# Kernel tuning notes

Hardware: AMD Instinct MI355X
Metric: run time of the kernel (lower is better)

Reference implementation:

```python
import jax, jax.numpy as jnp
import numpy as np

D = 1024        # d_model
H = 16          # query heads
HKV = 4         # kv heads (GQA)
HD = D // H     # head dim = 64
MAX_T = 1024
EPS = 1e-6
CAP = 50.0      # logit softcap


def _rope_cache(max_t, hd):
    inv = 1.0 / (10000.0 ** (np.arange(0, hd, 2, dtype=np.float32) / hd))  # (hd/2,)
    t = np.arange(max_t, dtype=np.float32)
    f = np.outer(t, inv)                                                   # (max_t, hd/2)
    return jnp.asarray(np.cos(f)), jnp.asarray(np.sin(f))


def setup_inputs() -> dict:
    key = jax.random.key(0)
    ks = jax.random.split(key, 5)
    x = jax.random.normal(ks[0], (2, 64, 256, D), jnp.float32)  # (B,T,S,D)
    wq = jax.random.normal(ks[1], (D, H * HD), jnp.float32) * 0.02
    wk = jax.random.normal(ks[2], (D, HKV * HD), jnp.float32) * 0.02
    wv = jax.random.normal(ks[3], (D, HKV * HD), jnp.float32) * 0.02
    wo = jax.random.normal(ks[4], (H * HD, D), jnp.float32) * 0.02
    q_scale = jnp.ones((HD,), jnp.float32)  # QKNorm learnable gains
    k_scale = jnp.ones((HD,), jnp.float32)
    rope_cos, rope_sin = _rope_cache(MAX_T, HD)
    return {"x": x, "wq": wq, "wk": wk, "wv": wv, "wo": wo,
            "q_scale": q_scale, "k_scale": k_scale,
            "rope_cos": rope_cos, "rope_sin": rope_sin}


def _rmsnorm(v, scale):
    return v * jax.lax.rsqrt(jnp.mean(v * v, axis=-1, keepdims=True) + EPS) * scale


def reference(x, wq, wk, wv, wo, q_scale, k_scale, rope_cos, rope_sin):
    B, T, S, Dm = x.shape
    # fold spatial positions into batch: each position attends causally over time
    xt = x.transpose(0, 2, 1, 3).reshape(B * S, T, Dm)          # (N,T,D)
    q = (xt @ wq).reshape(B * S, T, H, HD)
    k = (xt @ wk).reshape(B * S, T, HKV, HD)
    v = (xt @ wv).reshape(B * S, T, HKV, HD)
    # QK-norm (RMSNorm over head_dim) before RoPE
    q = _rmsnorm(q, q_scale)
    k = _rmsnorm(k, k_scale)
    # 1D RoPE over temporal positions (split-half convention)
    cos = rope_cos[:T][None, :, None, :]                        # (1,T,1,HD/2)
    sin = rope_sin[:T][None, :, None, :]

    def rot(u):
        u1, u2 = jnp.split(u, 2, axis=-1)
        return jnp.concatenate([u1 * cos - u2 * sin, u1 * sin + u2 * cos], axis=-1)

    q = rot(q)
    k = rot(k)
    # GQA: expand kv heads to match query heads
    rep = H // HKV
    k = jnp.repeat(k, rep, axis=2)
    v = jnp.repeat(v, rep, axis=2)
    scores = jnp.einsum('nthd,nshd->nhts', q, k) / np.float32(np.sqrt(HD))
    scores = CAP * jnp.tanh(scores / CAP)                        # logit softcap
    causal = jnp.tril(jnp.ones((T, T), bool))
    scores = jnp.where(causal, scores, jnp.float32(-1e30))
    a = jax.nn.softmax(scores, axis=-1)
    o = jnp.einsum('nhts,nshd->nthd', a, v).reshape(B * S, T, H * HD) @ wo
    return o.reshape(B, S, T, Dm).transpose(0, 2, 1, 3)          # (B,T,S,D)
```

## Files before the change

### kernel.cpp

```cpp
#include <hip/hip_runtime.h>
#include <hip/hip_bf16.h>

#define DM   1024
#define NHQ  16
#define NKVH 4
#define HDIM 64
#define TTT  64
#define SSS  256
#define NBB  2
#define MROWS 32768

using short8 = __attribute__((ext_vector_type(8))) short;
using short4v = __attribute__((ext_vector_type(4))) short;
using f32x4  = __attribute__((ext_vector_type(4))) float;

__device__ __forceinline__ short f2bf(float f) {
  union { __hip_bfloat16 h; short s; } u;
  u.h = __float2bfloat16(f);
  return u.s;
}

__device__ __forceinline__ f32x4 mfma16(short8 a, short8 b, f32x4 c) {
  return __builtin_amdgcn_mfma_f32_16x16x32_bf16(a, b, c, 0, 0, 0);
}

__device__ __forceinline__ void gload_lds16(const void* g, void* l) {
  __builtin_amdgcn_global_load_lds(
      (const __attribute__((address_space(1))) void*)g,
      (__attribute__((address_space(3))) void*)l, 16, 0, 0);
}

__global__ __launch_bounds__(256) void k_prep(const float* __restrict__ x,
                                              short* __restrict__ xb,
                                              const float* __restrict__ wq,
                                              const float* __restrict__ wk,
                                              const float* __restrict__ wv,
                                              const float* __restrict__ wo,
                                              short* __restrict__ wqkvT,
                                              short* __restrict__ woT) {
  __shared__ float tile[32][33];
  int bid = blockIdx.x;
  if (bid < 4096) {
    float4 v[8];
    #pragma unroll
    for (int i = 0; i < 8; ++i) {
      int r = bid * 8 + i;
      int n = r >> 6, t = r & 63;
      int b = n >> 8, s = n & 255;
      v[i] = ((const float4*)(x + ((size_t)((b * TTT + t) * SSS + s)) * DM))[threadIdx.x];
    }
    #pragma unroll
    for (int i = 0; i < 8; ++i) {
      int r = bid * 8 + i;
      short4 o;
      o.x = f2bf(v[i].x); o.y = f2bf(v[i].y); o.z = f2bf(v[i].z); o.w = f2bf(v[i].w);
      ((short4*)(xb + (size_t)r * DM))[threadIdx.x] = o;
    }
    return;
  }
  bid -= 4096;
  const float* w; short* wt; int cols;
  if (bid < 1024)      { w = wq; wt = wqkvT; cols = 1024; }
  else if (bid < 1280) { w = wk; wt = wqkvT + (size_t)1024 * 1024; cols = 256; bid -= 1024; }
  else if (bid < 1536) { w = wv; wt = wqkvT + (size_t)1280 * 1024; cols = 256; bid -= 1280; }
  else                 { w = wo; wt = woT; cols = 1024; bid -= 1536; }
  int ctiles = cols >> 5;
  int tj = bid % ctiles;
  int td = bid / ctiles;
  int lx = threadIdx.x & 31, ly = threadIdx.x >> 5;
  #pragma unroll
  for (int rr = 0; rr < 32; rr += 8)
    tile[rr + ly][lx] = w[(size_t)(td * 32 + rr + ly) * cols + tj * 32 + lx];
  __syncthreads();
  #pragma unroll
  for (int rr = 0; rr < 32; rr += 8)
    wt[(size_t)(tj * 32 + rr + ly) * 1024 + td * 32 + lx] = f2bf(tile[lx][rr + ly]);
}

#define TILE(RAK0, RAK1, RBK0, RBK1, NLB, CLB, G, IA, IB, VM)                  \
  {                                                                            \
    short8 a[4], b0[4], b1[4];                                                 \
    _Pragma("unroll") for (int n = 0; n < 4; ++n)                              \
        b0[n] = *(const short8*)(RBK0 + n * 1024);                             \
    _Pragma("unroll") for (int m = 0; m < 4; ++m)                              \
        a[m] = *(const short8*)(RAK0 + m * 1024);                              \
    if (IA) stA0(NLB, (G + 1) * 64);                                           \
    __builtin_amdgcn_s_barrier();                                              \
    asm volatile("s_waitcnt lgkmcnt(0)" ::: "memory");                         \
    __builtin_amdgcn_s_setprio(1);                                             \
    _Pragma("unroll") for (int m = 0; m < 4; ++m)                              \
      _Pragma("unroll") for (int n = 0; n < 4; ++n)                            \
          acc[m][n] = mfma16(a[m], b0[n], acc[m][n]);                          \
    __builtin_amdgcn_s_setprio(0);                                             \
    __builtin_amdgcn_s_barrier();                                              \
    _Pragma("unroll") for (int m = 0; m < 4; ++m)                              \
        a[m] = *(const short8*)(RAK0 + 4096 + m * 1024);                       \
    if (IA) stA1(NLB, (G + 1) * 64);                                           \
    __builtin_amdgcn_s_barrier();                                              \
    asm volatile("s_waitcnt lgkmcnt(0)" ::: "memory");                         \
    __builtin_amdgcn_s_setprio(1);                                             \
    _Pragma("unroll") for (int m = 0; m < 4; ++m)                              \
      _Pragma("unroll") for (int n = 0; n < 4; ++n)                            \
          acc[4 + m][n] = mfma16(a[m], b0[n], acc[4 + m][n]);                  \
    __builtin_amdgcn_s_setprio(0);                                             \
    __builtin_amdgcn_s_barrier();                                              \
    _Pragma("unroll") for (int n = 0; n < 4; ++n)                              \
        b1[n] = *(const short8*)(RBK1 + n * 1024);                             \
    _Pragma("unroll") for (int m = 0; m < 4; ++m)                              \
        a[m] = *(const short8*)(RAK1 + m * 1024);                              \
    __builtin_amdgcn_s_barrier();                                              \
    asm volatile("s_waitcnt lgkmcnt(0)" ::: "memory");                         \
    __builtin_amdgcn_s_setprio(1);                                             \
    _Pragma("unroll") for (int m = 0; m < 4; ++m)                              \
      _Pragma("unroll") for (int n = 0; n < 4; ++n)                            \
          acc[m][n] = mfma16(a[m], b1[n], acc[m][n]);                          \
    __builtin_amdgcn_s_setprio(0);                                             \
    __builtin_amdgcn_s_barrier();                                              \
    _Pragma("unroll") for (int m = 0; m < 4; ++m)                              \
        a[m] = *(const short8*)(RAK1 + 4096 + m * 1024);                       \
    if (IB) stB(CLB, (G + 2) * 64);                                            \
    __builtin_amdgcn_s_barrier();                                              \
    asm volatile("s_waitcnt lgkmcnt(0)" ::: "memory");                         \
    __builtin_amdgcn_s_setprio(1);                                             \
    _Pragma("unroll") for (int m = 0; m < 4; ++m)                              \
      _Pragma("unroll") for (int n = 0; n < 4; ++n)                            \
          acc[4 + m][n] = mfma16(a[m], b1[n], acc[4 + m][n]);                  \
    __builtin_amdgcn_s_setprio(0);                                             \
    if (VM == 4)      asm volatile("s_waitcnt vmcnt(4)" ::: "memory");         \
    else if (VM == 0) asm volatile("s_waitcnt vmcnt(0)" ::: "memory");         \
    __builtin_amdgcn_s_barrier();                                              \
  }

__device__ __forceinline__ void gemm256(const short* __restrict__ Ab,
                                        const short* __restrict__ Bb,
                                        short* __restrict__ sm,
                                        f32x4 (&acc)[8][4]) {
  const int tid = threadIdx.x, lane = tid & 63, wid = tid >> 6;
  const int wr = wid >> 2, wc = wid & 3;
  const int ln15 = lane & 15, lhi = lane >> 4;
  const int rsw = ln15 & 7;
  const int row_t = tid >> 3;
  const int sw = ((tid & 7) ^ (row_t & 7)) << 3;
  const short* pA0 = Ab + (size_t)row_t * 1024 + sw;
  const short* pA1 = pA0 + (size_t)64 * 1024;
  const short* pA2 = pA0 + (size_t)128 * 1024;
  const short* pA3 = pA0 + (size_t)192 * 1024;
  const short* pB0 = Bb + (size_t)row_t * 1024 + sw;
  const short* pB1 = pB0 + (size_t)64 * 1024;
  const short* pB2 = pB0 + (size_t)128 * 1024;
  const short* pB3 = pB0 + (size_t)192 * 1024;
  auto stA0 = [&](short* lb, int kt) {
    gload_lds16(pA0 + kt, lb + tid * 8);
    gload_lds16(pA1 + kt, lb + 4096 + tid * 8);
  };
  auto stA1 = [&](short* lb, int kt) {
    gload_lds16(pA2 + kt, lb + 8192 + tid * 8);
    gload_lds16(pA3 + kt, lb + 12288 + tid * 8);
  };
  auto stB = [&](short* lb, int kt) {
    gload_lds16(pB0 + kt, lb + 16384 + tid * 8);
    gload_lds16(pB1 + kt, lb + 20480 + tid * 8);
    gload_lds16(pB2 + kt, lb + 24576 + tid * 8);
    gload_lds16(pB3 + kt, lb + 28672 + tid * 8);
  };
  const int sk0 = (lhi ^ rsw) << 3;
  const int sk1 = ((4 + lhi) ^ rsw) << 3;
  const short* rA0k0 = sm + (wr * 128 + ln15) * 64 + sk0;
  const short* rA0k1 = sm + (wr * 128 + ln15) * 64 + sk1;
  const short* rB0k0 = sm + 16384 + (wc * 64 + ln15) * 64 + sk0;
  const short* rB0k1 = sm + 16384 + (wc * 64 + ln15) * 64 + sk1;
  const short* rA1k0 = rA0k0 + 32768;
  const short* rA1k1 = rA0k1 + 32768;
  const short* rB1k0 = rB0k0 + 32768;
  const short* rB1k1 = rB0k1 + 32768;
  short* buf0 = sm;
  short* buf1 = sm + 32768;
  stA0(buf0, 0); stA1(buf0, 0); stB(buf0, 0);
  stA0(buf1, 64); stA1(buf1, 64); stB(buf1, 64);
  asm volatile("s_waitcnt vmcnt(8)" ::: "memory");
  __builtin_amdgcn_s_barrier();
  TILE(rA0k0, rA0k1, rB0k0, rB0k1, buf1, buf0, 0, 0, 1, 4)
  TILE(rA1k0, rA1k1, rB1k0, rB1k1, buf0, buf1, 1, 1, 1, 4)
  for (int gg = 1; gg < 7; ++gg) {
    const int g0 = gg * 2;
    TILE(rA0k0, rA0k1, rB0k0, rB0k1, buf1, buf0, g0, 1, 1, 4)
    TILE(rA1k0, rA1k1, rB1k0, rB1k1, buf0, buf1, g0 + 1, 1, 1, 4)
  }
  TILE(rA0k0, rA0k1, rB0k0, rB0k1, buf1, buf0, 14, 1, 0, 0)
  TILE(rA1k0, rA1k1, rB1k0, rB1k1, buf0, buf1, 15, 0, 0, -1)
}

__global__ __launch_bounds__(512) void k_qkv(
    const short* __restrict__ xb, const short* __restrict__ wt,
    const float* __restrict__ qscale, const float* __restrict__ kscale,
    const float* __restrict__ rcos, const float* __restrict__ rsin,
    short* __restrict__ qb, short* __restrict__ kb, short* __restrict__ vb) {
  __shared__ __align__(16) short sm[65536];
  const int bid = blockIdx.x;
  const int swz = (bid & 7) * 96 + (bid >> 3);
  const int tn = swz % 6, tm = swz / 6;
  f32x4 acc[8][4] = {};
  gemm256(xb + (size_t)tm * 256 * 1024, wt + (size_t)tn * 256 * 1024, sm, acc);

  const int tid = threadIdx.x, lane = tid & 63, wid = tid >> 6;
  const int wr = wid >> 2, wc = wid & 3;
  const int ln15 = lane & 15, lhi = lane >> 4;
  short* ot = sm;
  if (tn < 5) {
    const float* scale = (tn < 4) ? qscale : kscale;
    float sc[4];
    #pragma unroll
    for (int n = 0; n < 4; ++n) sc[n] = scale[n * 16 + ln15];
    #pragma unroll
    for (int m = 0; m < 8; ++m) {
      #pragma unroll
      for (int j = 0; j < 4; ++j) {
        float ss = 0.f;
        #pragma unroll
        for (int n = 0; n < 4; ++n) { float v = acc[m][n][j]; ss += v * v; }
        #pragma unroll
        for (int off = 8; off; off >>= 1) ss += __shfl_xor(ss, off, 64);
        float rms = rsqrtf(ss * (1.f / 64.f) + 1e-6f);
        int rl = wr * 128 + m * 16 + lhi * 4 + j;
        int t = (tm * 256 + rl) & 63;
        #pragma unroll
        for (int n = 0; n < 2; ++n) {
          int i = n * 16 + ln15;
          float cs = rcos[t * 32 + i], sn = rsin[t * 32 + i];
          float v1 = acc[m][n][j] * rms * sc[n];
          float v2 = acc[m][n + 2][j] * rms * sc[n + 2];
          ot[rl * 256 + wc * 64 + i]      = f2bf(v1 * cs - v2 * sn);
          ot[rl * 256 + wc * 64 + i + 32] = f2bf(v1 * sn + v2 * cs);
        }
      }
    }
  } else {
    #pragma unroll
    for (int m = 0; m < 8; ++m)
      #pragma unroll
      for (int n = 0; n < 4; ++n)
        #pragma unroll
        for (int j = 0; j < 4; ++j) {
          int rl = wr * 128 + m * 16 + lhi * 4 + j;
          ot[rl * 256 + wc * 64 + n * 16 + ln15] = f2bf(acc[m][n][j]);
        }
  }
  __syncthreads();
  {
    int row = tid >> 1, half = tid & 1;
    int r = tm * 256 + row;
    const uint4* src = (const uint4*)(ot + row * 256 + half * 128);
    short* dst;
    if (tn < 4)       dst = qb + (size_t)r * 1024 + tn * 256 + half * 128;
    else if (tn == 4) dst = kb + (size_t)r * 256 + half * 128;
    else              dst = vb + (size_t)r * 256 + half * 128;
    uint4* d4 = (uint4*)dst;
    #pragma unroll
    for (int i = 0; i < 16; ++i) d4[i] = src[i];
  }
}

__global__ __launch_bounds__(512) void k_attn(const short* __restrict__ qb,
                                              const short* __restrict__ kb,
                                              const short* __restrict__ vb,
                                              short* __restrict__ ob) {
  __shared__ __align__(16) short Vt[2][256 * 72];
  __shared__ __align__(16) short Ps[8][64 * 72];
  const int n0 = blockIdx.x * 2;
  const int tid = threadIdx.x, lane = tid & 63, wid = tid >> 6;
  const int ln15 = lane & 15, lhi = lane >> 4;
  short8 vr0[4], vr1[4];
  {
    const short* vrow0 = vb + ((size_t)(n0 * 64 + lane)) * 256;
    const short* vrow1 = vrow0 + 64 * 256;
    #pragma unroll
    for (int i = 0; i < 4; ++i) vr1[i] = *(const short8*)(vrow1 + wid * 32 + i * 8);
    #pragma unroll
    for (int i = 0; i < 4; ++i) vr0[i] = *(const short8*)(vrow0 + wid * 32 + i * 8);
  }
  #pragma unroll
  for (int i = 0; i < 4; ++i) {
    int d = wid * 32 + i * 8;
    #pragma unroll
    for (int e = 0; e < 8; ++e) Vt[0][(d + e) * 72 + lane] = vr0[i][e];
  }
  short* Pt = &Ps[wid][0];
  #pragma unroll
  for (int ss = 0; ss < 2; ++ss) {
    const int n = n0 + ss;
    if (ss == 1) {
      #pragma unroll
      for (int i = 0; i < 4; ++i) {
        int d = wid * 32 + i * 8;
        #pragma unroll
        for (int e = 0; e < 8; ++e) Vt[1][(d + e) * 72 + lane] = vr1[i][e];
      }
    }
    short8 aq[2][4][2];
    #pragma unroll
    for (int hh = 0; hh < 2; ++hh)
      #pragma unroll
      for (int nn = 0; nn < 4; ++nn)
        #pragma unroll
        for (int kk = 0; kk < 2; ++kk)
          aq[hh][nn][kk] = *(const short8*)(qb + ((size_t)(n * 64 + nn * 16 + ln15)) * 1024
                                               + (wid + hh * 8) * 64 + kk * 32 + lhi * 8);
    __syncthreads();
    const short* Vts = &Vt[ss][0];
    #pragma unroll
    for (int hh = 0; hh < 2; ++hh) {
      const int h = wid + hh * 8;
      const int kvh = h >> 2;
      short8 bk[4][2];
      #pragma unroll
      for (int m = 0; m < 4; ++m)
        #pragma unroll
        for (int kk = 0; kk < 2; ++kk)
          bk[m][kk] = *(const short8*)(kb + ((size_t)(n * 64 + m * 16 + ln15)) * 256
                                          + kvh * 64 + kk * 32 + lhi * 8);
      f32x4 sa[4][4] = {};
      __builtin_amdgcn_s_setprio(1);
      #pragma unroll
      for (int kk = 0; kk < 2; ++kk)
        #pragma unroll
        for (int m = 0; m < 4; ++m)
          #pragma unroll
          for (int nn = 0; nn < 4; ++nn)
            sa[m][nn] = mfma16(bk[m][kk], aq[hh][nn][kk], sa[m][nn]);
      __builtin_amdgcn_s_setprio(0);
      #pragma unroll
      for (int m = 0; m < 4; ++m)
        #pragma unroll
        for (int nn = 0; nn < 4; ++nn)
          #pragma unroll
          for (int j = 0; j < 4; ++j) {
            float e2 = __expf(sa[m][nn][j] * 0.005f);
            float cap = 50.f * (e2 - 1.f) * __builtin_amdgcn_rcpf(e2 + 1.f);
            int scur = m * 16 + lhi * 4 + j, tcur = nn * 16 + ln15;
            sa[m][nn][j] = (scur <= tcur) ? cap : -1e30f;
          }
      float inv[4];
      #pragma unroll
      for (int nn = 0; nn < 4; ++nn) {
        float mx = -3e38f;
        #pragma unroll
        for (int m = 0; m < 4; ++m)
          #pragma unroll
          for (int j = 0; j < 4; ++j) mx = fmaxf(mx, sa[m][nn][j]);
        mx = fmaxf(mx, __shfl_xor(mx, 16, 64));
        mx = fmaxf(mx, __shfl_xor(mx, 32, 64));
        float sum = 0.f;
        #pragma unroll
        for (int m = 0; m < 4; ++m)
          #pragma unroll
          for (int j = 0; j < 4; ++j) {
            float e = __expf(sa[m][nn][j] - mx);
            sa[m][nn][j] = e; sum += e;
          }
        sum += __shfl_xor(sum, 16, 64);
        sum += __shfl_xor(sum, 32, 64);
        inv[nn] = __builtin_amdgcn_rcpf(sum);
      }
      #pragma unroll
      for (int nn = 0; nn < 4; ++nn)
        #pragma unroll
        for (int m = 0; m < 4; ++m) {
          short4v w;
          #pragma unroll
          for (int j = 0; j < 4; ++j) w[j] = f2bf(sa[m][nn][j] * inv[nn]);
          *(short4v*)(Pt + (nn * 16 + ln15) * 72 + m * 16 + lhi * 4) = w;
        }
      short8 ap[4][2], bv[4][2];
      #pragma unroll
      for (int m = 0; m < 4; ++m)
        #pragma unroll
        for (int kk = 0; kk < 2; ++kk)
          ap[m][kk] = *(const short8*)(Pt + (m * 16 + ln15) * 72 + kk * 32 + lhi * 8);
      #pragma unroll
      for (int nn = 0; nn < 4; ++nn)
        #pragma unroll
        for (int kk = 0; kk < 2; ++kk)
          bv[nn][kk] = *(const short8*)(Vts + (kvh * 64 + nn * 16 + ln15) * 72 + kk * 32 + lhi * 8);
      f32x4 oa[4][4] = {};
      __builtin_amdgcn_s_setprio(1);
      #pragma unroll
      for (int kk = 0; kk < 2; ++kk)
        #pragma unroll
        for (int m = 0; m < 4; ++m)
          #pragma unroll
          for (int nn = 0; nn < 4; ++nn)
            oa[m][nn] = mfma16(ap[m][kk], bv[nn][kk], oa[m][nn]);
      __builtin_amdgcn_s_setprio(0);
      #pragma unroll
      for (int m = 0; m < 4; ++m)
        #pragma unroll
        for (int nn = 0; nn < 4; ++nn)
          #pragma unroll
          for (int j = 0; j < 4; ++j)
            Pt[(m * 16 + lhi * 4 + j) * 72 + nn * 16 + ln15] = f2bf(oa[m][nn][j]);
      #pragma unroll
      for (int c = 0; c < 8; ++c)
        *(uint4*)(ob + ((size_t)(n * 64 + lane)) * 1024 + h * 64 + c * 8)
            = *(const uint4*)(Pt + lane * 72 + c * 8);
    }
  }
}

__global__ __launch_bounds__(512) void k_out(const short* __restrict__ ab,
                                             const short* __restrict__ wt,
                                             float* __restrict__ out) {
  __shared__ __align__(16) short sm[65536];
  const int bid = blockIdx.x;
  const int swz = (bid & 7) * 64 + (bid >> 3);
  const int tn = swz & 3, tm = swz >> 2;
  f32x4 acc[8][4] = {};
  gemm256(ab + (size_t)tm * 256 * 1024, wt + (size_t)tn * 256 * 1024, sm, acc);

  const int tid = threadIdx.x, lane = tid & 63, wid = tid >> 6;
  const int wr = wid >> 2, wc = wid & 3;
  const int ln15 = lane & 15, lhi = lane >> 4;
  float* of = (float*)sm;
  #pragma unroll
  for (int ch = 0; ch < 2; ++ch) {
    if (wr == ch) {
      #pragma unroll
      for (int m = 0; m < 8; ++m)
        #pragma unroll
        for (int n = 0; n < 4; ++n)
          #pragma unroll
          for (int j = 0; j < 4; ++j)
            of[(m * 16 + lhi * 4 + j) * 256 + wc * 64 + n * 16 + ln15] = acc[m][n][j];
    }
    __syncthreads();
    {
      int row = tid >> 2, q4 = tid & 3;
      int r = tm * 256 + ch * 128 + row;
      int nseq = r >> 6, t = r & 63;
      int b = nseq >> 8, s = nseq & 255;
      float* dst = out + ((size_t)((b * TTT + t) * SSS + s)) * DM + tn * 256 + q4 * 64;
      const float4* src = (const float4*)(of + row * 256 + q4 * 64);
      float4* d4 = (float4*)dst;
      #pragma unroll
      for (int i = 0; i < 16; ++i) d4[i] = src[i];
    }
    __syncthreads();
  }
}

extern "C" void kernel_launch(void* const* d_in, const int* in_sizes, int n_in,
                              void* d_out, int out_size, void* d_ws, size_t ws_size,
                              hipStream_t stream) {
  const float* x  = (const float*)d_in[0];
  const float* wq = (const float*)d_in[1];
  const float* wk = (const float*)d_in[2];
  const float* wv = (const float*)d_in[3];
  const float* wo = (const float*)d_in[4];
  const float* qs = (const float*)d_in[5];
  const float* ks = (const float*)d_in[6];
  const float* rc = (const float*)d_in[7];
  const float* rs = (const float*)d_in[8];
  float* out = (float*)d_out;
  char* ws = (char*)d_ws;

  short* xb    = (short*)(ws);
  short* wqkvT = (short*)(ws + 67108864);
  short* woT   = (short*)(ws + 70254592);
  short* qb    = (short*)(ws + 72351744);
  short* kb    = (short*)(ws + 139460608);
  short* vb    = (short*)(ws + 156237824);
  short* ob    = xb;

  k_prep<<<6656, 256, 0, stream>>>(x, xb, wq, wk, wv, wo, wqkvT, woT);
  k_qkv<<<768, 512, 0, stream>>>(xb, wqkvT, qs, ks, rc, rs, qb, kb, vb);
  k_attn<<<256, 512, 0, stream>>>(qb, kb, vb, ob);
  k_out<<<512, 512, 0, stream>>>(ob, woT, out);
}
```

Measured before the change: 318.8 us.

## Make QKV and output GEMMs persistent with cross-tile prefetch overlapping epilogue

The QKV and output projection kernels become persistent: 256 blocks each loop over 3 (QKV) or 2 (out) 256x256 tiles. During the last K-steps of one tile they prefetch the first K-slices of the next tile into the free LDS buffer, and the epilogue runs in chunks through the upper half of LDS. This hides the GEMM pipeline ramp-up and the epilogue behind loads and removes the launch tail of the earlier 768/512-block grids. In exchange the epilogue needs more barriers, and with only 256 blocks some of the GPU's CUs (256 on MI355X per public docs) may sit idle.

```diff
diff --git a/kernel.cpp b/kernel.cpp
--- a/kernel.cpp
+++ b/kernel.cpp
@@ -77,14 +77,49 @@
     wt[(size_t)(tj * 32 + rr + ly) * 1024 + td * 32 + lx] = f2bf(tile[lx][rr + ly]);
 }
 
-#define TILE(RAK0, RAK1, RBK0, RBK1, NLB, CLB, G, IA, IB, VM)                  \
+#define GEMM_SETUP                                                             \
+  const int tid = threadIdx.x, lane = tid & 63, wid = tid >> 6;                \
+  const int wr = wid >> 2, wc = wid & 3;                                       \
+  const int ln15 = lane & 15, lhi = lane >> 4;                                 \
+  const int rsw = ln15 & 7;                                                    \
+  const size_t goff = (size_t)(tid >> 3) * 1024                                \
+                    + (size_t)(((tid & 7) ^ ((tid >> 3) & 7)) << 3);           \
+  auto stA0 = [&](short* lb, const short* base, int kt) {                      \
+    gload_lds16(base + goff + kt, lb + tid * 8);                               \
+    gload_lds16(base + goff + 65536 + kt, lb + 4096 + tid * 8);                \
+  };                                                                           \
+  auto stA1 = [&](short* lb, const short* base, int kt) {                      \
+    gload_lds16(base + goff + 131072 + kt, lb + 8192 + tid * 8);               \
+    gload_lds16(base + goff + 196608 + kt, lb + 12288 + tid * 8);              \
+  };                                                                           \
+  auto stB = [&](short* lb, const short* base, int kt) {                       \
+    gload_lds16(base + goff + kt, lb + 16384 + tid * 8);                       \
+    gload_lds16(base + goff + 65536 + kt, lb + 20480 + tid * 8);               \
+    gload_lds16(base + goff + 131072 + kt, lb + 24576 + tid * 8);              \
+    gload_lds16(base + goff + 196608 + kt, lb + 28672 + tid * 8);              \
+  };                                                                           \
+  const int sk0 = (lhi ^ rsw) << 3;                                            \
+  const int sk1 = ((4 + lhi) ^ rsw) << 3;                                      \
+  const short* rA0k0 = sm + (wr * 128 + ln15) * 64 + sk0;                      \
+  const short* rA0k1 = sm + (wr * 128 + ln15) * 64 + sk1;                      \
+  const short* rB0k0 = sm + 16384 + (wc * 64 + ln15) * 64 + sk0;               \
+  const short* rB0k1 = sm + 16384 + (wc * 64 + ln15) * 64 + sk1;               \
+  const short* rA1k0 = rA0k0 + 32768;                                          \
+  const short* rA1k1 = rA0k1 + 32768;                                          \
+  const short* rB1k0 = rB0k0 + 32768;                                          \
+  const short* rB1k1 = rB0k1 + 32768;                                          \
+  short* buf0 = sm;                                                            \
+  short* buf1 = sm + 32768;                                                    \
+  f32x4 acc[8][4] = {};
+
+#define PTILE(RAK0, RAK1, RBK0, RBK1, NLB, CLB, IA, ABASE, AKT, IB, BBASE, BKT, VM) \
   {                                                                            \
     short8 a[4], b0[4], b1[4];                                                 \
     _Pragma("unroll") for (int n = 0; n < 4; ++n)                              \
         b0[n] = *(const short8*)(RBK0 + n * 1024);                             \
     _Pragma("unroll") for (int m = 0; m < 4; ++m)                              \
         a[m] = *(const short8*)(RAK0 + m * 1024);                              \
-    if (IA) stA0(NLB, (G + 1) * 64);                                           \
+    if (IA) stA0(NLB, ABASE, AKT);                                             \
     __builtin_amdgcn_s_barrier();                                              \
     asm volatile("s_waitcnt lgkmcnt(0)" ::: "memory");                         \
     __builtin_amdgcn_s_setprio(1);                                             \
@@ -95,7 +130,7 @@
     __builtin_amdgcn_s_barrier();                                              \
     _Pragma("unroll") for (int m = 0; m < 4; ++m)                              \
         a[m] = *(const short8*)(RAK0 + 4096 + m * 1024);                       \
-    if (IA) stA1(NLB, (G + 1) * 64);                                           \
+    if (IA) stA1(NLB, ABASE, AKT);                                             \
     __builtin_amdgcn_s_barrier();                                              \
     asm volatile("s_waitcnt lgkmcnt(0)" ::: "memory");                         \
     __builtin_amdgcn_s_setprio(1);                                             \
@@ -118,7 +153,7 @@
     __builtin_amdgcn_s_barrier();                                              \
     _Pragma("unroll") for (int m = 0; m < 4; ++m)                              \
         a[m] = *(const short8*)(RAK1 + 4096 + m * 1024);                       \
-    if (IB) stB(CLB, (G + 2) * 64);                                            \
+    if (IB) stB(CLB, BBASE, BKT);                                              \
     __builtin_amdgcn_s_barrier();                                              \
     asm volatile("s_waitcnt lgkmcnt(0)" ::: "memory");                         \
     __builtin_amdgcn_s_setprio(1);                                             \
@@ -126,69 +161,24 @@
       _Pragma("unroll") for (int n = 0; n < 4; ++n)                            \
           acc[4 + m][n] = mfma16(a[m], b1[n], acc[4 + m][n]);                  \
     __builtin_amdgcn_s_setprio(0);                                             \
-    if (VM == 4)      asm volatile("s_waitcnt vmcnt(4)" ::: "memory");         \
-    else if (VM == 0) asm volatile("s_waitcnt vmcnt(0)" ::: "memory");         \
-    __builtin_amdgcn_s_barrier();                                              \
-  }
-
-__device__ __forceinline__ void gemm256(const short* __restrict__ Ab,
-                                        const short* __restrict__ Bb,
-                                        short* __restrict__ sm,
-                                        f32x4 (&acc)[8][4]) {
-  const int tid = threadIdx.x, lane = tid & 63, wid = tid >> 6;
-  const int wr = wid >> 2, wc = wid & 3;
-  const int ln15 = lane & 15, lhi = lane >> 4;
-  const int rsw = ln15 & 7;
-  const int row_t = tid >> 3;
-  const int sw = ((tid & 7) ^ (row_t & 7)) << 3;
-  const short* pA0 = Ab + (size_t)row_t * 1024 + sw;
-  const short* pA1 = pA0 + (size_t)64 * 1024;
-  const short* pA2 = pA0 + (size_t)128 * 1024;
-  const short* pA3 = pA0 + (size_t)192 * 1024;
-  const short* pB0 = Bb + (size_t)row_t * 1024 + sw;
-  const short* pB1 = pB0 + (size_t)64 * 1024;
-  const short* pB2 = pB0 + (size_t)128 * 1024;
-  const short* pB3 = pB0 + (size_t)192 * 1024;
-  auto stA0 = [&](short* lb, int kt) {
-    gload_lds16(pA0 + kt, lb + tid * 8);
-    gload_lds16(pA1 + kt, lb + 4096 + tid * 8);
-  };
-  auto stA1 = [&](short* lb, int kt) {
-    gload_lds16(pA2 + kt, lb + 8192 + tid * 8);
-    gload_lds16(pA3 + kt, lb + 12288 + tid * 8);
-  };
-  auto stB = [&](short* lb, int kt) {
-    gload_lds16(pB0 + kt, lb + 16384 + tid * 8);
-    gload_lds16(pB1 + kt, lb + 20480 + tid * 8);
-    gload_lds16(pB2 + kt, lb + 24576 + tid * 8);
-    gload_lds16(pB3 + kt, lb + 28672 + tid * 8);
-  };
-  const int sk0 = (lhi ^ rsw) << 3;
-  const int sk1 = ((4 + lhi) ^ rsw) << 3;
-  const short* rA0k0 = sm + (wr * 128 + ln15) * 64 + sk0;
-  const short* rA0k1 = sm + (wr * 128 + ln15) * 64 + sk1;
-  const short* rB0k0 = sm + 16384 + (wc * 64 + ln15) * 64 + sk0;
-  const short* rB0k1 = sm + 16384 + (wc * 64 + ln15) * 64 + sk1;
-  const short* rA1k0 = rA0k0 + 32768;
-  const short* rA1k1 = rA0k1 + 32768;
-  const short* rB1k0 = rB0k0 + 32768;
-  const short* rB1k1 = rB0k1 + 32768;
-  short* buf0 = sm;
-  short* buf1 = sm + 32768;
-  stA0(buf0, 0); stA1(buf0, 0); stB(buf0, 0);
-  stA0(buf1, 64); stA1(buf1, 64); stB(buf1, 64);
-  asm volatile("s_waitcnt vmcnt(8)" ::: "memory");
-  __builtin_amdgcn_s_barrier();
-  TILE(rA0k0, rA0k1, rB0k0, rB0k1, buf1, buf0, 0, 0, 1, 4)
-  TILE(rA1k0, rA1k1, rB1k0, rB1k1, buf0, buf1, 1, 1, 1, 4)
-  for (int gg = 1; gg < 7; ++gg) {
-    const int g0 = gg * 2;
-    TILE(rA0k0, rA0k1, rB0k0, rB0k1, buf1, buf0, g0, 1, 1, 4)
-    TILE(rA1k0, rA1k1, rB1k0, rB1k1, buf0, buf1, g0 + 1, 1, 1, 4)
-  }
-  TILE(rA0k0, rA0k1, rB0k0, rB0k1, buf1, buf0, 14, 1, 0, 0)
-  TILE(rA1k0, rA1k1, rB1k0, rB1k1, buf0, buf1, 15, 0, 0, -1)
-}
+    if ((VM) == 4)      asm volatile("s_waitcnt vmcnt(4)" ::: "memory");       \
+    else if ((VM) == 0) asm volatile("s_waitcnt vmcnt(0)" ::: "memory");       \
+    __builtin_amdgcn_s_barrier();                                              \
+  }
+
+#define PGEMM_TILES(MORE, AC, BC, AN, BN)                                      \
+  PTILE(rA0k0, rA0k1, rB0k0, rB0k1, buf1, buf0, (j > 0), AC, 64, true, BC, 128, 4) \
+  PTILE(rA1k0, rA1k1, rB1k0, rB1k1, buf0, buf1, true, AC, 128, true, BC, 192, 4)   \
+  for (int gg = 1; gg < 7; ++gg) {                                             \
+    PTILE(rA0k0, rA0k1, rB0k0, rB0k1, buf1, buf0, true, AC, (2 * gg + 1) * 64, \
+          true, BC, (2 * gg + 2) * 64, 4)                                      \
+    PTILE(rA1k0, rA1k1, rB1k0, rB1k1, buf0, buf1, true, AC, (2 * gg + 2) * 64, \
+          true, BC, (2 * gg + 3) * 64, 4)                                      \
+  }                                                                            \
+  PTILE(rA0k0, rA0k1, rB0k0, rB0k1, buf1, buf0, true, AC, 960, (MORE), BN, 0,  \
+        (MORE) ? 4 : 0)                                                        \
+  PTILE(rA1k0, rA1k1, rB1k0, rB1k1, buf0, buf1, (MORE), AN, 0, (MORE), BN, 64, \
+        (MORE) ? 4 : -1)
 
 __global__ __launch_bounds__(512) void k_qkv(
     const short* __restrict__ xb, const short* __restrict__ wt,
@@ -197,66 +187,104 @@
     short* __restrict__ qb, short* __restrict__ kb, short* __restrict__ vb) {
   __shared__ __align__(16) short sm[65536];
   const int bid = blockIdx.x;
-  const int swz = (bid & 7) * 96 + (bid >> 3);
-  const int tn = swz % 6, tm = swz / 6;
-  f32x4 acc[8][4] = {};
-  gemm256(xb + (size_t)tm * 256 * 1024, wt + (size_t)tn * 256 * 1024, sm, acc);
-
-  const int tid = threadIdx.x, lane = tid & 63, wid = tid >> 6;
-  const int wr = wid >> 2, wc = wid & 3;
-  const int ln15 = lane & 15, lhi = lane >> 4;
-  short* ot = sm;
-  if (tn < 5) {
-    const float* scale = (tn < 4) ? qscale : kscale;
-    float sc[4];
-    #pragma unroll
-    for (int n = 0; n < 4; ++n) sc[n] = scale[n * 16 + ln15];
-    #pragma unroll
-    for (int m = 0; m < 8; ++m) {
-      #pragma unroll
-      for (int j = 0; j < 4; ++j) {
-        float ss = 0.f;
-        #pragma unroll
-        for (int n = 0; n < 4; ++n) { float v = acc[m][n][j]; ss += v * v; }
-        #pragma unroll
-        for (int off = 8; off; off >>= 1) ss += __shfl_xor(ss, off, 64);
-        float rms = rsqrtf(ss * (1.f / 64.f) + 1e-6f);
-        int rl = wr * 128 + m * 16 + lhi * 4 + j;
-        int t = (tm * 256 + rl) & 63;
-        #pragma unroll
-        for (int n = 0; n < 2; ++n) {
-          int i = n * 16 + ln15;
-          float cs = rcos[t * 32 + i], sn = rsin[t * 32 + i];
-          float v1 = acc[m][n][j] * rms * sc[n];
-          float v2 = acc[m][n + 2][j] * rms * sc[n + 2];
-          ot[rl * 256 + wc * 64 + i]      = f2bf(v1 * cs - v2 * sn);
-          ot[rl * 256 + wc * 64 + i + 32] = f2bf(v1 * sn + v2 * cs);
+  GEMM_SETUP
+  short* epi = sm + 32768;
+  int swz = (bid & 7) * 96 + (bid >> 3);
+  int tn = swz % 6, tm = swz / 6;
+  const short* Ac = xb + (size_t)tm * 262144;
+  const short* Bc = wt + (size_t)tn * 262144;
+  stA0(buf0, Ac, 0); stA1(buf0, Ac, 0); stB(buf0, Bc, 0);
+  stA0(buf1, Ac, 64); stA1(buf1, Ac, 64); stB(buf1, Bc, 64);
+  asm volatile("s_waitcnt vmcnt(8)" ::: "memory");
+  __builtin_amdgcn_s_barrier();
+  for (int j = 0; j < 3; ++j) {
+    const bool more = (j < 2);
+    int swzn = (bid & 7) * 96 + (j + 1) * 32 + (bid >> 3);
+    int tnn = swzn % 6, tmn = swzn / 6;
+    const short* An = more ? (xb + (size_t)tmn * 262144) : Ac;
+    const short* Bn = more ? (wt + (size_t)tnn * 262144) : Bc;
+    PGEMM_TILES(more, Ac, Bc, An, Bn)
+    if (tn < 5) {
+      const float* scale = (tn < 4) ? qscale : kscale;
+      float sc[4];
+      #pragma unroll
+      for (int n = 0; n < 4; ++n) sc[n] = scale[n * 16 + ln15];
+      #pragma unroll
+      for (int p = 0; p < 4; ++p) {
+        if (wr == (p >> 1)) {
+          #pragma unroll
+          for (int mm = 0; mm < 4; ++mm) {
+            const int m = (p & 1) * 4 + mm;
+            #pragma unroll
+            for (int jj = 0; jj < 4; ++jj) {
+              float ss = 0.f;
+              #pragma unroll
+              for (int n = 0; n < 4; ++n) { float v = acc[m][n][jj]; ss += v * v; }
+              #pragma unroll
+              for (int off = 8; off; off >>= 1) ss += __shfl_xor(ss, off, 64);
+              float rms = rsqrtf(ss * (1.f / 64.f) + 1e-6f);
+              int t = mm * 16 + lhi * 4 + jj;
+              #pragma unroll
+              for (int n = 0; n < 2; ++n) {
+                int i = n * 16 + ln15;
+                float cs = rcos[t * 32 + i], sn = rsin[t * 32 + i];
+                float v1 = acc[m][n][jj] * rms * sc[n];
+                float v2 = acc[m][n + 2][jj] * rms * sc[n + 2];
+                epi[t * 256 + wc * 64 + i]      = f2bf(v1 * cs - v2 * sn);
+                epi[t * 256 + wc * 64 + i + 32] = f2bf(v1 * sn + v2 * cs);
+              }
+            }
+          }
         }
+        asm volatile("s_waitcnt lgkmcnt(0)" ::: "memory");
+        __builtin_amdgcn_s_barrier();
+        {
+          int row = tid >> 3, seg = tid & 7;
+          int r = tm * 256 + p * 64 + row;
+          const uint4* src = (const uint4*)(epi + row * 256 + seg * 32);
+          short* dst = (tn < 4) ? (qb + (size_t)r * 1024 + tn * 256 + seg * 32)
+                                : (kb + (size_t)r * 256 + seg * 32);
+          uint4* d4 = (uint4*)dst;
+          #pragma unroll
+          for (int i2 = 0; i2 < 4; ++i2) d4[i2] = src[i2];
+        }
+        __builtin_amdgcn_s_barrier();
       }
-    }
-  } else {
-    #pragma unroll
-    for (int m = 0; m < 8; ++m)
-      #pragma unroll
-      for (int n = 0; n < 4; ++n)
-        #pragma unroll
-        for (int j = 0; j < 4; ++j) {
-          int rl = wr * 128 + m * 16 + lhi * 4 + j;
-          ot[rl * 256 + wc * 64 + n * 16 + ln15] = f2bf(acc[m][n][j]);
+    } else {
+      #pragma unroll
+      for (int p = 0; p < 4; ++p) {
+        if (wr == (p >> 1)) {
+          #pragma unroll
+          for (int mm = 0; mm < 4; ++mm) {
+            const int m = (p & 1) * 4 + mm;
+            #pragma unroll
+            for (int n = 0; n < 4; ++n)
+              #pragma unroll
+              for (int jj = 0; jj < 4; ++jj)
+                epi[(mm * 16 + lhi * 4 + jj) * 256 + wc * 64 + n * 16 + ln15]
+                    = f2bf(acc[m][n][jj]);
+          }
         }
-  }
-  __syncthreads();
-  {
-    int row = tid >> 1, half = tid & 1;
-    int r = tm * 256 + row;
-    const uint4* src = (const uint4*)(ot + row * 256 + half * 128);
-    short* dst;
-    if (tn < 4)       dst = qb + (size_t)r * 1024 + tn * 256 + half * 128;
-    else if (tn == 4) dst = kb + (size_t)r * 256 + half * 128;
-    else              dst = vb + (size_t)r * 256 + half * 128;
-    uint4* d4 = (uint4*)dst;
-    #pragma unroll
-    for (int i = 0; i < 16; ++i) d4[i] = src[i];
+        asm volatile("s_waitcnt lgkmcnt(0)" ::: "memory");
+        __builtin_amdgcn_s_barrier();
+        {
+          int row = tid >> 3, seg = tid & 7;
+          int r = tm * 256 + p * 64 + row;
+          uint4* d4 = (uint4*)(vb + (size_t)r * 256 + seg * 32);
+          const uint4* src = (const uint4*)(epi + row * 256 + seg * 32);
+          #pragma unroll
+          for (int i2 = 0; i2 < 4; ++i2) d4[i2] = src[i2];
+        }
+        __builtin_amdgcn_s_barrier();
+      }
+    }
+    if (more) {
+      #pragma unroll
+      for (int m = 0; m < 8; ++m)
+        #pragma unroll
+        for (int n = 0; n < 4; ++n) acc[m][n] = (f32x4){0.f, 0.f, 0.f, 0.f};
+      Ac = An; Bc = Bn; tm = tmn; tn = tnn;
+    }
   }
 }
 
@@ -411,39 +439,58 @@
                                              float* __restrict__ out) {
   __shared__ __align__(16) short sm[65536];
   const int bid = blockIdx.x;
-  const int swz = (bid & 7) * 64 + (bid >> 3);
-  const int tn = swz & 3, tm = swz >> 2;
-  f32x4 acc[8][4] = {};
-  gemm256(ab + (size_t)tm * 256 * 1024, wt + (size_t)tn * 256 * 1024, sm, acc);
-
-  const int tid = threadIdx.x, lane = tid & 63, wid = tid >> 6;
-  const int wr = wid >> 2, wc = wid & 3;
-  const int ln15 = lane & 15, lhi = lane >> 4;
-  float* of = (float*)sm;
-  #pragma unroll
-  for (int ch = 0; ch < 2; ++ch) {
-    if (wr == ch) {
+  GEMM_SETUP
+  float* epif = (float*)(sm + 32768);
+  int swz = (bid & 7) * 64 + (bid >> 3);
+  int tn = swz & 3, tm = swz >> 2;
+  const short* Ac = ab + (size_t)tm * 262144;
+  const short* Bc = wt + (size_t)tn * 262144;
+  stA0(buf0, Ac, 0); stA1(buf0, Ac, 0); stB(buf0, Bc, 0);
+  stA0(buf1, Ac, 64); stA1(buf1, Ac, 64); stB(buf1, Bc, 64);
+  asm volatile("s_waitcnt vmcnt(8)" ::: "memory");
+  __builtin_amdgcn_s_barrier();
+  for (int j = 0; j < 2; ++j) {
+    const bool more = (j < 1);
+    int swzn = (bid & 7) * 64 + 32 + (bid >> 3);
+    int tnn = swzn & 3, tmn = swzn >> 2;
+    const short* An = more ? (ab + (size_t)tmn * 262144) : Ac;
+    const short* Bn = more ? (wt + (size_t)tnn * 262144) : Bc;
+    PGEMM_TILES(more, Ac, Bc, An, Bn)
+    #pragma unroll
+    for (int p = 0; p < 8; ++p) {
+      if (wr == (p >> 2)) {
+        #pragma unroll
+        for (int mm = 0; mm < 2; ++mm) {
+          const int m = (p & 3) * 2 + mm;
+          #pragma unroll
+          for (int n = 0; n < 4; ++n)
+            #pragma unroll
+            for (int jj = 0; jj < 4; ++jj)
+              epif[(mm * 16 + lhi * 4 + jj) * 256 + wc * 64 + n * 16 + ln15]
+                  = acc[m][n][jj];
+        }
+      }
+      asm volatile("s_waitcnt lgkmcnt(0)" ::: "memory");
+      __builtin_amdgcn_s_barrier();
+      {
+        int row = tid >> 4, seg = tid & 15;
+        int r = tm * 256 + p * 32 + row;
+        int nseq = r >> 6, t = r & 63;
+        int b = nseq >> 8, s = nseq & 255;
+        float* dst = out + ((size_t)((b * TTT + t) * SSS + s)) * DM + tn * 256 + seg * 16;
+        const float4* src = (const float4*)(epif + row * 256 + seg * 16);
+        #pragma unroll
+        for (int i2 = 0; i2 < 4; ++i2) ((float4*)dst)[i2] = src[i2];
+      }
+      __builtin_amdgcn_s_barrier();
+    }
+    if (more) {
       #pragma unroll
       for (int m = 0; m < 8; ++m)
         #pragma unroll
-        for (int n = 0; n < 4; ++n)
-          #pragma unroll
-          for (int j = 0; j < 4; ++j)
-            of[(m * 16 + lhi * 4 + j) * 256 + wc * 64 + n * 16 + ln15] = acc[m][n][j];
-    }
-    __syncthreads();
-    {
-      int row = tid >> 2, q4 = tid & 3;
-      int r = tm * 256 + ch * 128 + row;
-      int nseq = r >> 6, t = r & 63;
-      int b = nseq >> 8, s = nseq & 255;
-      float* dst = out + ((size_t)((b * TTT + t) * SSS + s)) * DM + tn * 256 + q4 * 64;
-      const float4* src = (const float4*)(of + row * 256 + q4 * 64);
-      float4* d4 = (float4*)dst;
-      #pragma unroll
-      for (int i = 0; i < 16; ++i) d4[i] = src[i];
-    }
-    __syncthreads();
+        for (int n = 0; n < 4; ++n) acc[m][n] = (f32x4){0.f, 0.f, 0.f, 0.f};
+      Ac = An; Bc = Bn; tm = tmn; tn = tnn;
+    }
   }
 }
 
@@ -471,7 +518,7 @@
   short* ob    = xb;
 
   k_prep<<<6656, 256, 0, stream>>>(x, xb, wq, wk, wv, wo, wqkvT, woT);
-  k_qkv<<<768, 512, 0, stream>>>(xb, wqkvT, qs, ks, rc, rs, qb, kb, vb);
+  k_qkv<<<256, 512, 0, stream>>>(xb, wqkvT, qs, ks, rc, rs, qb, kb, vb);
   k_attn<<<256, 512, 0, stream>>>(qb, kb, vb, ob);
-  k_out<<<512, 512, 0, stream>>>(ob, woT, out);
-}
+  k_out<<<256, 512, 0, stream>>>(ob, woT, out);
+}
```

Result: slower. 429.7 us (+34.8%).
